# Kernel tuning notes

Measured on AMD Instinct MI355X. Metric: run time of the kernel, lower is better.

## Reference

```python
import jax, jax.numpy as jnp
from jax import lax
import numpy as np

B = 2048
N = 10  # wires on q_device0
C64 = jnp.complex64

# fixed gate matrices (qubit ordering matches wire-list order)
S_ = jnp.array([[1, 0], [0, 1j]], C64)
T_ = jnp.array([[1, 0], [0, np.exp(1j * np.pi / 4)]], C64)
SX_ = 0.5 * jnp.array([[1 + 1j, 1 - 1j], [1 - 1j, 1 + 1j]], C64)
Y_ = jnp.array([[0, -1j], [1j, 0]], C64)
CNOT_ = jnp.array([[1, 0, 0, 0], [0, 1, 0, 0], [0, 0, 0, 1], [0, 0, 1, 0]], C64)
CZ_ = jnp.diag(jnp.array([1, 1, 1, -1], C64))
CY_ = jnp.array([[1, 0, 0, 0], [0, 1, 0, 0], [0, 0, 0, -1j], [0, 0, 1j, 0]], C64)
SWAP_ = jnp.array([[1, 0, 0, 0], [0, 0, 1, 0], [0, 1, 0, 0], [0, 0, 0, 1]], C64)
_cs = np.eye(8); _cs[[5, 6]] = _cs[[6, 5]]  # CSWAP: |101> <-> |110>
CSWAP_ = jnp.array(_cs, C64)
_tf = np.eye(8); _tf[[6, 7]] = _tf[[7, 6]]  # Toffoli: |110> <-> |111>
TOFF_ = jnp.array(_tf, C64)

# parametrized single-qubit gate builders; t scalar -> [2,2], t [B] -> [B,2,2]
def _rx(t):
    c = jnp.cos(t / 2).astype(C64)
    s = -1j * jnp.sin(t / 2).astype(C64)
    return jnp.stack([jnp.stack([c, s], -1), jnp.stack([s, c], -1)], -2)

def _ry(t):
    c = jnp.cos(t / 2).astype(C64)
    s = jnp.sin(t / 2).astype(C64)
    return jnp.stack([jnp.stack([c, -s], -1), jnp.stack([s, c], -1)], -2)

def _rz(t):
    a = jnp.exp(-0.5j * t.astype(C64))
    b = jnp.exp(0.5j * t.astype(C64))
    z = jnp.zeros_like(a)
    return jnp.stack([jnp.stack([a, z], -1), jnp.stack([z, b], -1)], -2)

def _phase(t):
    e = jnp.exp(1j * t.astype(C64))
    o = jnp.ones_like(e)
    z = jnp.zeros_like(e)
    return jnp.stack([jnp.stack([o, z], -1), jnp.stack([z, e], -1)], -2)

def _rot(phi, th, om):  # RZ(om) RY(th) RZ(phi), pennylane/torchquantum convention
    c = jnp.cos(th / 2).astype(C64)
    s = jnp.sin(th / 2).astype(C64)
    p = phi.astype(C64); w = om.astype(C64)
    m00 = jnp.exp(-0.5j * (p + w)) * c
    m01 = -jnp.exp(0.5j * (p - w)) * s
    m10 = jnp.exp(-0.5j * (p - w)) * s
    m11 = jnp.exp(0.5j * (p + w)) * c
    return jnp.stack([jnp.stack([m00, m01], -1), jnp.stack([m10, m11], -1)], -2)

def _apply1(psi, U, w):  # psi: [B]+(2,)*N, U: [2,2] or [B,2,2]
    s = jnp.moveaxis(psi, w + 1, 1)
    if U.ndim == 2:
        s = jnp.einsum('ij,bj...->bi...', U, s)
    else:
        s = jnp.einsum('bij,bj...->bi...', U, s)
    return jnp.moveaxis(s, 1, w + 1)

def _applyk(psi, U, wires):  # fixed k-qubit gate, U: [2^k, 2^k]
    k = len(wires)
    axes = tuple(w + 1 for w in wires)
    s = jnp.moveaxis(psi, axes, tuple(range(1, k + 1)))
    sh = s.shape
    s = s.reshape((sh[0], 2 ** k) + sh[k + 1:])
    s = jnp.einsum('ij,bj...->bi...', U, s)
    return jnp.moveaxis(s.reshape(sh), tuple(range(1, k + 1)), axes)

def _forward(x, conv1_w, conv1_b, conv2_w, conv2_b, fc1_w, fc1_b, fc2_w, fc2_b,
             theta0, theta_rz, theta_ps, rot_p):
    dn = ('NCHW', 'OIHW', 'NCHW')
    h = lax.conv_general_dilated(x, conv1_w, (1, 1), 'VALID', dimension_numbers=dn)
    h = jax.nn.relu(h + conv1_b[None, :, None, None])
    h = lax.conv_general_dilated(h, conv2_w, (1, 1), 'VALID', dimension_numbers=dn)
    h = jax.nn.relu(h + conv2_b[None, :, None, None])
    h = lax.reduce_window(h, -jnp.inf, lax.max, (1, 1, 2, 2), (1, 1, 2, 2), 'VALID')
    h = h.reshape(h.shape[0], -1)  # [B, 9216], dropout = identity (eval)
    h = jax.nn.relu(h @ fc1_w.T + fc1_b)
    a = jax.nn.sigmoid(h @ fc2_w.T + fc2_b) * (2.0 * np.pi)  # angles [B, 10]
    bsz = a.shape[0]
    psi = jnp.zeros((bsz, 2 ** N), C64).at[:, 0].set(1.0).reshape((bsz,) + (2,) * N)
    trz = jnp.reshape(theta_rz, ())
    tps = jnp.reshape(theta_ps, ())
    for k in range(N):                      # TrainableRxAll
        psi = _apply1(psi, _rx(theta0[k]), k)
    for k in range(N):                      # RxAll with input angles
        psi = _apply1(psi, _rx(a[:, k]), k)
    psi = _apply1(psi, _rx(a[:, 1]), 1)
    psi = _apply1(psi, _rx(jnp.asarray(-np.pi / 4, jnp.float32)), 5)  # q_layer2 fixed
    psi = _apply1(psi, _ry(a[:, 2]), 2)
    psi = _apply1(psi, _rz(a[:, 3]), 3)
    psi = _apply1(psi, S_, 4)
    psi = _apply1(psi, T_, 5)
    psi = _apply1(psi, _rz(trz), 6)         # q_layer3
    psi = _apply1(psi, SX_, 7)
    # (q_device1 ops on a separate 3-wire device do not affect the output)
    psi = _applyk(psi, CZ_, (0, 5))
    psi = _applyk(psi, CNOT_, (0, 5))
    psi = _applyk(psi, CY_, (0, 5))
    psi = _applyk(psi, CY_, (3, 8))         # q_layer4
    psi = _applyk(psi, SWAP_, (2, 3))
    psi = _applyk(psi, CSWAP_, (4, 5, 6))
    psi = _applyk(psi, TOFF_, (8, 5, 0))    # q_layer5
    psi = _apply1(psi, _phase(tps), 8)      # q_layer6
    psi = _apply1(psi, _phase(a[:, 7]), 7)
    psi = _apply1(psi, _rot(rot_p[0], rot_p[1], rot_p[2]), 4)  # q_layer7
    psi = _apply1(psi, _rot(a[:, 6], a[:, 7], a[:, 8]), 5)
    axes = tuple(range(1, N + 1))
    evs = [jnp.real(jnp.sum(jnp.conj(psi) * _apply1(psi, Y_, k), axis=axes))
           for k in range(N)]
    ev = jnp.stack(evs, -1)                 # [B, 10] <Y_k>
    return jax.nn.log_softmax(ev, axis=1)


def setup_inputs() -> dict:
    key = jax.random.key(0)
    ks = jax.random.split(key, 13)
    return {
        'x': jax.random.normal(ks[0], (B, 1, 28, 28), jnp.float32),
        'conv1_w': jax.random.normal(ks[1], (32, 1, 3, 3), jnp.float32) * 0.2,
        'conv1_b': jnp.zeros((32,), jnp.float32),
        'conv2_w': jax.random.normal(ks[2], (64, 32, 3, 3), jnp.float32) * 0.05,
        'conv2_b': jnp.zeros((64,), jnp.float32),
        'fc1_w': jax.random.normal(ks[3], (128, 9216), jnp.float32) * 0.01,
        'fc1_b': jnp.zeros((128,), jnp.float32),
        'fc2_w': jax.random.normal(ks[4], (10, 128), jnp.float32) * 0.1,
        'fc2_b': jnp.zeros((10,), jnp.float32),
        'theta0': jax.random.normal(ks[5], (10,), jnp.float32),
        'theta_rz': jax.random.normal(ks[6], (1,), jnp.float32),
        'theta_ps': jax.random.normal(ks[7], (1,), jnp.float32),
        'rot_p': jax.random.normal(ks[8], (3,), jnp.float32),
    }


def reference(x, conv1_w, conv1_b, conv2_w, conv2_b, fc1_w, fc1_b, fc2_w, fc2_b,
              theta0, theta_rz, theta_ps, rot_p):
    return _forward(x, conv1_w, conv1_b, conv2_w, conv2_b, fc1_w, fc1_b, fc2_w, fc2_b,
                    theta0, theta_rz, theta_ps, rot_p)
```

## Files before the change

kernel.cpp:

```cpp
#include <hip/hip_runtime.h>
#include <math.h>

typedef short short8 __attribute__((ext_vector_type(8)));
typedef float f32x4 __attribute__((ext_vector_type(4)));
typedef float f32x16 __attribute__((ext_vector_type(16)));

#define GLB_CP(p) ((const __attribute__((address_space(1))) void*)(p))
#define LDS_CP(p) ((__attribute__((address_space(3))) void*)(p))

__device__ __forceinline__ float2 cmul(float2 a, float2 b) {
    return make_float2(a.x * b.x - a.y * b.y, a.x * b.y + a.y * b.x);
}

__device__ __forceinline__ ushort f2bf(float f) {
    uint u = __float_as_uint(f);
    uint r = (u + 0x7FFFu + ((u >> 16) & 1u)) >> 16;
    return (ushort)r;
}

__global__ __launch_bounds__(256) void prep_kernel(
    const float* __restrict__ c2w, const float* __restrict__ f1w,
    ushort* __restrict__ wt2, ushort* __restrict__ wf1)
{
    int i = blockIdx.x * 256 + threadIdx.x;
    if (i < 18432) {
        int icl = i & 7;
        int t = i >> 3;
        int oc = t & 63;
        int t2 = t >> 6;
        int icg = t2 & 3;
        int tap = t2 >> 2;
        int ic = icg * 8 + icl;
        wt2[i] = f2bf(c2w[(oc * 32 + ic) * 9 + tap]);
    } else if (i < 18432 + 1179648) {
        int j = i - 18432;
        wf1[j] = f2bf(f1w[j]);
    }
}

__global__ __launch_bounds__(256) void conv1_kernel(
    const float* __restrict__ x, const float* __restrict__ w1,
    const float* __restrict__ b1, ushort* __restrict__ h1b)
{
    __shared__ float wl[288];
    __shared__ float bl[32];
    int tid = threadIdx.x;
    for (int e = tid; e < 288; e += 256) wl[e] = w1[e];
    if (tid < 32) bl[tid] = b1[tid];
    __syncthreads();
    int e = blockIdx.x * 256 + tid;
    int icg = e & 3;
    int t = e >> 2;
    int pix = t % 676;
    int b = t / 676;
    int y = pix / 26, xc = pix % 26;
    const float* xp = x + b * 784 + y * 28 + xc;
    float in9[9];
#pragma unroll
    for (int ky = 0; ky < 3; ++ky)
#pragma unroll
        for (int kx = 0; kx < 3; ++kx) in9[ky * 3 + kx] = xp[ky * 28 + kx];
    short8 outv;
#pragma unroll
    for (int o = 0; o < 8; ++o) {
        int oc = icg * 8 + o;
        float acc = bl[oc];
#pragma unroll
        for (int k = 0; k < 9; ++k) acc = fmaf(in9[k], wl[oc * 9 + k], acc);
        outv[o] = (short)f2bf(fmaxf(acc, 0.f));
    }
    *(short8*)&h1b[((b * 4 + icg) * 676 + pix) * 8] = outv;
}

__global__ __launch_bounds__(384, 3) void conv2_img(
    const ushort* __restrict__ h1b, const ushort* __restrict__ wt2,
    const float* __restrict__ c2b, ushort* __restrict__ pooled)
{
    __shared__ __attribute__((aligned(16))) ushort wt_lds[18432];
    __shared__ __attribute__((aligned(16))) ushort in_lds[2][8704];
    int b = blockIdx.x;
    int tid = threadIdx.x;
    int wave = tid >> 6;
    int lane = tid & 63;
    int lo = lane & 31;
    int hi = lane >> 5;

    for (int c = wave; c < 36; c += 6) {
        const ushort* src = wt2 + (size_t)(c * 64 + lane) * 8;
        __builtin_amdgcn_global_load_lds(GLB_CP(src), LDS_CP(wt_lds + c * 512), 16, 0, 0);
    }
    {
        const ushort* base = h1b + (size_t)b * 21632;
        for (int c = wave; c < 17; c += 6) {
            int e = c * 64 + lane;
            if (e > 1039) e = 1039;
            int icg = e / 260;
            int rem = e - icg * 260;
            const ushort* src = base + ((size_t)icg * 676 + rem) * 8;
            __builtin_amdgcn_global_load_lds(GLB_CP(src), LDS_CP(in_lds[0] + c * 512), 16, 0, 0);
        }
    }
    float bias0 = c2b[lo];
    float bias1 = c2b[lo + 32];
    __syncthreads();

    int rx = wave % 3, ry = wave / 3;
    int xcoord = rx * 8 + (lo & 7);
    int ycoord = ry * 4 + (lo >> 3);
    int pbase = ycoord * 26 + xcoord;
    ushort* pout = pooled + (size_t)b * 9216;
    int pcolb = rx * 4 + 2 * hi;

#pragma unroll
    for (int band = 0; band < 3; ++band) {
        if (band < 2) {
            const ushort* base = h1b + (size_t)b * 21632 + (size_t)(band + 1) * 8 * 26 * 8;
            ushort* dst = in_lds[(band + 1) & 1];
            for (int c = wave; c < 17; c += 6) {
                int e = c * 64 + lane;
                if (e > 1039) e = 1039;
                int icg = e / 260;
                int rem = e - icg * 260;
                const ushort* src = base + ((size_t)icg * 676 + rem) * 8;
                __builtin_amdgcn_global_load_lds(GLB_CP(src), LDS_CP(dst + c * 512), 16, 0, 0);
            }
        }

        const ushort* ib = in_lds[band & 1];
        f32x16 acc0 = (f32x16)0.f, acc1 = (f32x16)0.f;
#pragma unroll
        for (int tap = 0; tap < 9; ++tap) {
            int off = (tap / 3) * 26 + (tap % 3);
#pragma unroll
            for (int ks = 0; ks < 2; ++ks) {
                short8 bf = *(const short8*)&ib[((ks * 2 + hi) * 260 + pbase + off) * 8];
                short8 a0 = *(const short8*)&wt_lds[((tap * 4 + ks * 2 + hi) * 64 + lo) * 8];
                short8 a1 = *(const short8*)&wt_lds[((tap * 4 + ks * 2 + hi) * 64 + 32 + lo) * 8];
                acc0 = __builtin_amdgcn_mfma_f32_32x32x16_bf16(bf, a0, acc0, 0, 0, 0);
                acc1 = __builtin_amdgcn_mfma_f32_32x32x16_bf16(bf, a1, acc1, 0, 0, 0);
            }
        }

#pragma unroll
        for (int q = 0; q < 2; ++q) {
            int prow = band * 4 + ry * 2 + q;
            int base = 8 * q;
            float m00 = fmaxf(fmaxf(acc0[base], acc0[base + 1]), fmaxf(acc0[base + 4], acc0[base + 5]));
            float m01 = fmaxf(fmaxf(acc0[base + 2], acc0[base + 3]), fmaxf(acc0[base + 6], acc0[base + 7]));
            uint pk0 = (uint)f2bf(fmaxf(m00 + bias0, 0.f)) | ((uint)f2bf(fmaxf(m01 + bias0, 0.f)) << 16);
            *(uint*)&pout[lo * 144 + prow * 12 + pcolb] = pk0;
            float m10 = fmaxf(fmaxf(acc1[base], acc1[base + 1]), fmaxf(acc1[base + 4], acc1[base + 5]));
            float m11 = fmaxf(fmaxf(acc1[base + 2], acc1[base + 3]), fmaxf(acc1[base + 6], acc1[base + 7]));
            uint pk1 = (uint)f2bf(fmaxf(m10 + bias1, 0.f)) | ((uint)f2bf(fmaxf(m11 + bias1, 0.f)) << 16);
            *(uint*)&pout[(lo + 32) * 144 + prow * 12 + pcolb] = pk1;
        }
        __syncthreads();
    }
}

__global__ __launch_bounds__(256) void fc1_mfma(
    const ushort* __restrict__ pooled, const ushort* __restrict__ wf1,
    float* __restrict__ part)
{
    int bx = blockIdx.x, by = blockIdx.y;
    int tid = threadIdx.x;
    int wid = tid >> 6, lane = tid & 63;
    int lo = lane & 15, hi = lane >> 4;
    int m0 = bx * 32;
    int kb = by * 2304;

    f32x4 acc[2][2];
#pragma unroll
    for (int mt = 0; mt < 2; ++mt)
#pragma unroll
        for (int j = 0; j < 2; ++j) acc[mt][j] = (f32x4)0.f;

    const ushort* arow0 = pooled + (size_t)(m0 + lo) * 9216 + kb + hi * 8;
    const ushort* arow1 = arow0 + 16 * 9216;
    const ushort* brow0 = wf1 + (size_t)(wid * 32 + lo) * 9216 + kb + hi * 8;
    const ushort* brow1 = brow0 + 16 * 9216;

    for (int kt = 0; kt < 72; ++kt) {
        short8 a0 = *(const short8*)(arow0 + kt * 32);
        short8 a1 = *(const short8*)(arow1 + kt * 32);
        short8 b0 = *(const short8*)(brow0 + kt * 32);
        short8 b1 = *(const short8*)(brow1 + kt * 32);
        acc[0][0] = __builtin_amdgcn_mfma_f32_16x16x32_bf16(a0, b0, acc[0][0], 0, 0, 0);
        acc[1][0] = __builtin_amdgcn_mfma_f32_16x16x32_bf16(a1, b0, acc[1][0], 0, 0, 0);
        acc[0][1] = __builtin_amdgcn_mfma_f32_16x16x32_bf16(a0, b1, acc[0][1], 0, 0, 0);
        acc[1][1] = __builtin_amdgcn_mfma_f32_16x16x32_bf16(a1, b1, acc[1][1], 0, 0, 0);
    }
    float* pp = part + (size_t)by * 262144;
#pragma unroll
    for (int mt = 0; mt < 2; ++mt)
#pragma unroll
        for (int j = 0; j < 2; ++j)
#pragma unroll
            for (int r = 0; r < 4; ++r)
                pp[(m0 + mt * 16 + hi * 4 + r) * 128 + wid * 32 + j * 16 + lo] = acc[mt][j][r];
}

__global__ __launch_bounds__(256) void fc1_reduce_kernel(
    const float* __restrict__ part, const float* __restrict__ bias,
    float* __restrict__ outp)
{
    int idx = blockIdx.x * 256 + threadIdx.x;
    float s = 0.f;
#pragma unroll
    for (int ks = 0; ks < 4; ++ks) s += part[ks * 262144 + idx];
    outp[idx] = fmaxf(s + bias[idx & 127], 0.f);
}

__global__ __launch_bounds__(256) void fc2_kernel(
    const float* __restrict__ h, const float* __restrict__ w,
    const float* __restrict__ bias, float* __restrict__ ang)
{
    int idx = blockIdx.x * 256 + threadIdx.x;
    if (idx >= 20480) return;
    int b = idx / 10, n = idx % 10;
    const float* hp = h + b * 128;
    const float* wp = w + n * 128;
    float s = bias[n];
    for (int k = 0; k < 128; ++k) s = fmaf(hp[k], wp[k], s);
    ang[idx] = 6.28318530718f / (1.f + expf(-s));
}

__device__ __forceinline__ void apply_rot(float2* s, int p, float phi, float th,
                                          float om, int tid)
{
    float c, sn; sincosf(0.5f * th, &sn, &c);
    float A = 0.5f * (phi + om), Bv = 0.5f * (phi - om);
    float cA, sA; sincosf(A, &sA, &cA);
    float cB, sB; sincosf(Bv, &sB, &cB);
    float2 m00 = make_float2(cA * c, -sA * c);
    float2 m01 = make_float2(-cB * sn, -sB * sn);
    float2 m10 = make_float2(cB * sn, -sB * sn);
    float2 m11 = make_float2(cA * c, sA * c);
    for (int q = tid; q < 512; q += 256) {
        int i0 = ((q >> p) << (p + 1)) | (q & ((1 << p) - 1));
        int i1 = i0 | (1 << p);
        float2 aa = s[i0], bb = s[i1];
        s[i0] = make_float2(m00.x * aa.x - m00.y * aa.y + m01.x * bb.x - m01.y * bb.y,
                            m00.x * aa.y + m00.y * aa.x + m01.x * bb.y + m01.y * bb.x);
        s[i1] = make_float2(m10.x * aa.x - m10.y * aa.y + m11.x * bb.x - m11.y * bb.y,
                            m10.x * aa.y + m10.y * aa.x + m11.x * bb.y + m11.y * bb.x);
    }
}

__global__ __launch_bounds__(256) void quantum_kernel(
    const float* __restrict__ ang, const float* __restrict__ theta0,
    const float* __restrict__ theta_rz, const float* __restrict__ theta_ps,
    const float* __restrict__ rot_p, float* __restrict__ out)
{
    __shared__ float2 s[1024];
    __shared__ float red[40];
    int b = blockIdx.x;
    int tid = threadIdx.x;

    float a[10];
#pragma unroll
    for (int k = 0; k < 10; ++k) a[k] = ang[b * 10 + k];
    float th[10];
#pragma unroll
    for (int k = 0; k < 10; ++k) th[k] = theta0[k] + a[k];
    th[1] += a[1];
    th[5] -= 0.78539816339745f;

    float2 v[10][2];
#pragma unroll
    for (int k = 0; k < 10; ++k) {
        float c, sn; sincosf(0.5f * th[k], &sn, &c);
        v[k][0] = make_float2(c, 0.f);
        v[k][1] = make_float2(0.f, -sn);
    }
    { float c, sn; sincosf(0.5f * a[2], &sn, &c);
      float2 v0 = v[2][0], v1 = v[2][1];
      v[2][0] = make_float2(c * v0.x - sn * v1.x, c * v0.y - sn * v1.y);
      v[2][1] = make_float2(sn * v0.x + c * v1.x, sn * v0.y + c * v1.y); }
    { float c, sn; sincosf(0.5f * a[3], &sn, &c);
      v[3][0] = cmul(v[3][0], make_float2(c, -sn));
      v[3][1] = cmul(v[3][1], make_float2(c, sn)); }
    { float2 t = v[4][1]; v[4][1] = make_float2(-t.y, t.x); }
    { const float r = 0.70710678118655f;
      float2 t = v[5][1]; v[5][1] = make_float2(r * (t.x - t.y), r * (t.x + t.y)); }
    { float c, sn; sincosf(0.5f * theta_rz[0], &sn, &c);
      v[6][0] = cmul(v[6][0], make_float2(c, -sn));
      v[6][1] = cmul(v[6][1], make_float2(c, sn)); }
    { float2 p = v[7][0], q = v[7][1];
      v[7][0] = make_float2(0.5f * ((p.x - p.y) + (q.x + q.y)),
                            0.5f * ((p.x + p.y) + (q.y - q.x)));
      v[7][1] = make_float2(0.5f * ((p.x + p.y) + (q.x - q.y)),
                            0.5f * ((p.y - p.x) + (q.x + q.y))); }

    for (int i = tid; i < 1024; i += 256) {
        float2 c = ((i >> 9) & 1) ? v[0][1] : v[0][0];
#pragma unroll
        for (int k = 1; k < 10; ++k) {
            float2 vk = ((i >> (9 - k)) & 1) ? v[k][1] : v[k][0];
            c = cmul(c, vk);
        }
        s[i] = c;
    }
    __syncthreads();

    for (int i = tid; i < 1024; i += 256)
        if (((i >> 9) & 1) && ((i >> 4) & 1)) { s[i].x = -s[i].x; s[i].y = -s[i].y; }
    __syncthreads();
    { int j = tid;
      int i0 = 512 | ((j >> 4) << 5) | (j & 15);
      int i1 = i0 | 16;
      float2 t0 = s[i0], t1 = s[i1];
      s[i0] = t1; s[i1] = t0; }
    __syncthreads();
    { int j = tid;
      int i0 = 512 | ((j >> 4) << 5) | (j & 15);
      int i1 = i0 | 16;
      float2 t0 = s[i0], t1 = s[i1];
      s[i0] = make_float2(t1.y, -t1.x);
      s[i1] = make_float2(-t0.y, t0.x); }
    __syncthreads();
    { int j = tid;
      int i0 = (j & 1) | (((j >> 1) & 15) << 2) | (((j >> 5) & 7) << 7) | 64;
      int i1 = i0 | 2;
      float2 t0 = s[i0], t1 = s[i1];
      s[i0] = make_float2(t1.y, -t1.x);
      s[i1] = make_float2(-t0.y, t0.x); }
    __syncthreads();
    { int j = tid;
      int i0 = (j & 63) | 128 | (((j >> 6) & 3) << 8);
      int i1 = i0 ^ 0xC0;
      float2 t0 = s[i0], t1 = s[i1];
      s[i0] = t1; s[i1] = t0; }
    __syncthreads();
    if (tid < 128) {
      int j = tid;
      int i0 = (j & 7) | 16 | 32 | (((j >> 3) & 15) << 6);
      int i1 = i0 ^ 0x18;
      float2 t0 = s[i0], t1 = s[i1];
      s[i0] = t1; s[i1] = t0; }
    __syncthreads();
    if (tid < 128) {
      int j = tid;
      int i0 = (j & 1) | 2 | (((j >> 1) & 3) << 2) | 16 | (((j >> 3) & 15) << 5);
      int i1 = i0 | 512;
      float2 t0 = s[i0], t1 = s[i1];
      s[i0] = t1; s[i1] = t0; }
    __syncthreads();
    { float c1, s1; sincosf(theta_ps[0], &s1, &c1);
      float c2, s2; sincosf(a[7], &s2, &c2);
      float2 p1 = make_float2(c1, s1), p2 = make_float2(c2, s2);
      for (int i = tid; i < 1024; i += 256) {
          float2 t = s[i];
          if ((i >> 1) & 1) t = cmul(t, p1);
          if ((i >> 2) & 1) t = cmul(t, p2);
          s[i] = t;
      } }
    __syncthreads();
    apply_rot(s, 5, rot_p[0], rot_p[1], rot_p[2], tid);
    __syncthreads();
    apply_rot(s, 4, a[6], a[7], a[8], tid);
    __syncthreads();

    int wave = tid >> 6;
    for (int k = 0; k < 10; ++k) {
        int p = 9 - k;
        float part = 0.f;
        for (int q = tid; q < 512; q += 256) {
            int i0 = ((q >> p) << (p + 1)) | (q & ((1 << p) - 1));
            int i1 = i0 | (1 << p);
            float2 aa = s[i0], bb = s[i1];
            part += aa.x * bb.y - aa.y * bb.x;
        }
        part *= 2.f;
#pragma unroll
        for (int off = 32; off > 0; off >>= 1)
            part += __shfl_down(part, off, 64);
        if ((tid & 63) == 0) red[k * 4 + wave] = part;
    }
    __syncthreads();
    if (tid == 0) {
        float ev[10];
        float mx = -1e30f;
#pragma unroll
        for (int k = 0; k < 10; ++k) {
            ev[k] = red[k * 4] + red[k * 4 + 1] + red[k * 4 + 2] + red[k * 4 + 3];
            mx = fmaxf(mx, ev[k]);
        }
        float sum = 0.f;
#pragma unroll
        for (int k = 0; k < 10; ++k) sum += expf(ev[k] - mx);
        float lse = mx + logf(sum);
#pragma unroll
        for (int k = 0; k < 10; ++k) out[b * 10 + k] = ev[k] - lse;
    }
}

extern "C" void kernel_launch(void* const* d_in, const int* in_sizes, int n_in,
                              void* d_out, int out_size, void* d_ws, size_t ws_size,
                              hipStream_t stream)
{
    (void)in_sizes; (void)n_in; (void)out_size; (void)ws_size;
    const float* x    = (const float*)d_in[0];
    const float* c1w  = (const float*)d_in[1];
    const float* c1b  = (const float*)d_in[2];
    const float* c2w  = (const float*)d_in[3];
    const float* c2b  = (const float*)d_in[4];
    const float* f1w  = (const float*)d_in[5];
    const float* f1b  = (const float*)d_in[6];
    const float* f2w  = (const float*)d_in[7];
    const float* f2b  = (const float*)d_in[8];
    const float* th0  = (const float*)d_in[9];
    const float* trz  = (const float*)d_in[10];
    const float* tps  = (const float*)d_in[11];
    const float* rotp = (const float*)d_in[12];
    float* out = (float*)d_out;

    char* ws = (char*)d_ws;
    ushort* h1b    = (ushort*)(ws);
    ushort* pooled = (ushort*)(ws + 88604672);
    ushort* wt2    = (ushort*)(ws + 126353408);
    ushort* wf1    = (ushort*)(ws + 126390272);
    float*  part   = (float*)(ws + 128749568);
    float*  fc1o   = (float*)(ws + 132943872);
    float*  ang    = (float*)(ws + 133992448);

    prep_kernel<<<4680, 256, 0, stream>>>(c2w, f1w, wt2, wf1);
    conv1_kernel<<<21632, 256, 0, stream>>>(x, c1w, c1b, h1b);
    conv2_img<<<2048, 384, 0, stream>>>(h1b, wt2, c2b, pooled);
    fc1_mfma<<<dim3(64, 4), 256, 0, stream>>>(pooled, wf1, part);
    fc1_reduce_kernel<<<1024, 256, 0, stream>>>(part, f1b, fc1o);
    fc2_kernel<<<80, 256, 0, stream>>>(fc1o, f2w, f2b, ang);
    quantum_kernel<<<2048, 256, 0, stream>>>(ang, th0, trz, tps, rotp, out);
}
```

Before: 161.0 us.

## Make conv2 persistent over 8 images per block with whole-image LDS tiles

The conv2 kernel now launches 256 blocks that each loop over 8 images, loading the weights into LDS once per block instead of once per image. Each iteration double-buffers a full 26x26x32 input image, in place of three row bands, and each wave computes three 32-pixel tiles so the weight fragments it reads are reused across six MFMAs. This cuts repeated weight loads and per-band synchronisation, but uses more LDS and more accumulator registers (occupancy hint drops to 2). It also leaves 256 blocks to cover the whole GPU, which may underfill the CUs.

```diff
diff --git a/kernel.cpp b/kernel.cpp
--- a/kernel.cpp
+++ b/kernel.cpp
@@ -72,13 +72,31 @@
     *(short8*)&h1b[((b * 4 + icg) * 676 + pix) * 8] = outv;
 }
 
-__global__ __launch_bounds__(384, 3) void conv2_img(
+#define EPILOG(ACC0, ACC1, RX, RY)                                                         \
+    {                                                                                      \
+        int pcolb = (RX) * 4 + 2 * hi;                                                     \
+        _Pragma("unroll")                                                                  \
+        for (int q = 0; q < 2; ++q) {                                                      \
+            int prow = (RY) * 2 + q;                                                       \
+            int bs = 8 * q;                                                                \
+            float m00 = fmaxf(fmaxf(ACC0[bs], ACC0[bs + 1]), fmaxf(ACC0[bs + 4], ACC0[bs + 5])); \
+            float m01 = fmaxf(fmaxf(ACC0[bs + 2], ACC0[bs + 3]), fmaxf(ACC0[bs + 6], ACC0[bs + 7])); \
+            uint pk0 = (uint)f2bf(fmaxf(m00 + bias0, 0.f)) | ((uint)f2bf(fmaxf(m01 + bias0, 0.f)) << 16); \
+            *(uint*)&pout[lo * 144 + prow * 12 + pcolb] = pk0;                             \
+            float m10 = fmaxf(fmaxf(ACC1[bs], ACC1[bs + 1]), fmaxf(ACC1[bs + 4], ACC1[bs + 5])); \
+            float m11 = fmaxf(fmaxf(ACC1[bs + 2], ACC1[bs + 3]), fmaxf(ACC1[bs + 6], ACC1[bs + 7])); \
+            uint pk1 = (uint)f2bf(fmaxf(m10 + bias1, 0.f)) | ((uint)f2bf(fmaxf(m11 + bias1, 0.f)) << 16); \
+            *(uint*)&pout[(lo + 32) * 144 + prow * 12 + pcolb] = pk1;                      \
+        }                                                                                  \
+    }
+
+__global__ __launch_bounds__(384, 2) void conv2_persist(
     const ushort* __restrict__ h1b, const ushort* __restrict__ wt2,
     const float* __restrict__ c2b, ushort* __restrict__ pooled)
 {
     __shared__ __attribute__((aligned(16))) ushort wt_lds[18432];
-    __shared__ __attribute__((aligned(16))) ushort in_lds[2][8704];
-    int b = blockIdx.x;
+    __shared__ __attribute__((aligned(16))) ushort in_lds[2][22016];
+    int cu = blockIdx.x;
     int tid = threadIdx.x;
     int wave = tid >> 6;
     int lane = tid & 63;
@@ -90,70 +108,73 @@
         __builtin_amdgcn_global_load_lds(GLB_CP(src), LDS_CP(wt_lds + c * 512), 16, 0, 0);
     }
     {
-        const ushort* base = h1b + (size_t)b * 21632;
-        for (int c = wave; c < 17; c += 6) {
+        const ushort* base = h1b + (size_t)(cu * 8) * 21632;
+        for (int c = wave; c < 43; c += 6) {
             int e = c * 64 + lane;
-            if (e > 1039) e = 1039;
-            int icg = e / 260;
-            int rem = e - icg * 260;
-            const ushort* src = base + ((size_t)icg * 676 + rem) * 8;
-            __builtin_amdgcn_global_load_lds(GLB_CP(src), LDS_CP(in_lds[0] + c * 512), 16, 0, 0);
+            if (e > 2703) e = 2703;
+            __builtin_amdgcn_global_load_lds(GLB_CP(base + (size_t)e * 8),
+                                             LDS_CP(in_lds[0] + c * 512), 16, 0, 0);
         }
     }
     float bias0 = c2b[lo];
     float bias1 = c2b[lo + 32];
     __syncthreads();
 
-    int rx = wave % 3, ry = wave / 3;
-    int xcoord = rx * 8 + (lo & 7);
-    int ycoord = ry * 4 + (lo >> 3);
-    int pbase = ycoord * 26 + xcoord;
-    ushort* pout = pooled + (size_t)b * 9216;
-    int pcolb = rx * 4 + 2 * hi;
-
-#pragma unroll
-    for (int band = 0; band < 3; ++band) {
-        if (band < 2) {
-            const ushort* base = h1b + (size_t)b * 21632 + (size_t)(band + 1) * 8 * 26 * 8;
-            ushort* dst = in_lds[(band + 1) & 1];
-            for (int c = wave; c < 17; c += 6) {
+    int pb[3];
+#pragma unroll
+    for (int i = 0; i < 3; ++i) {
+        int r = wave + 6 * i;
+        int rx = r % 3, ry = r / 3;
+        int xcoord = rx * 8 + (lo & 7);
+        int ycoord = ry * 4 + (lo >> 3);
+        pb[i] = ycoord * 26 + xcoord;
+    }
+    int rx0 = wave % 3, ry0 = wave / 3;
+    int rx1 = (wave + 6) % 3, ry1 = (wave + 6) / 3;
+    int rx2 = (wave + 12) % 3, ry2 = (wave + 12) / 3;
+
+    for (int j = 0; j < 8; ++j) {
+        if (j < 7) {
+            const ushort* base = h1b + (size_t)(cu * 8 + j + 1) * 21632;
+            ushort* dst = in_lds[(j + 1) & 1];
+            for (int c = wave; c < 43; c += 6) {
                 int e = c * 64 + lane;
-                if (e > 1039) e = 1039;
-                int icg = e / 260;
-                int rem = e - icg * 260;
-                const ushort* src = base + ((size_t)icg * 676 + rem) * 8;
-                __builtin_amdgcn_global_load_lds(GLB_CP(src), LDS_CP(dst + c * 512), 16, 0, 0);
+                if (e > 2703) e = 2703;
+                __builtin_amdgcn_global_load_lds(GLB_CP(base + (size_t)e * 8),
+                                                 LDS_CP(dst + c * 512), 16, 0, 0);
             }
         }
 
-        const ushort* ib = in_lds[band & 1];
-        f32x16 acc0 = (f32x16)0.f, acc1 = (f32x16)0.f;
+        const ushort* ib = in_lds[j & 1];
+        f32x16 aA0 = (f32x16)0.f, aA1 = (f32x16)0.f;
+        f32x16 aB0 = (f32x16)0.f, aB1 = (f32x16)0.f;
+        f32x16 aC0 = (f32x16)0.f, aC1 = (f32x16)0.f;
+
 #pragma unroll
         for (int tap = 0; tap < 9; ++tap) {
             int off = (tap / 3) * 26 + (tap % 3);
 #pragma unroll
             for (int ks = 0; ks < 2; ++ks) {
-                short8 bf = *(const short8*)&ib[((ks * 2 + hi) * 260 + pbase + off) * 8];
-                short8 a0 = *(const short8*)&wt_lds[((tap * 4 + ks * 2 + hi) * 64 + lo) * 8];
-                short8 a1 = *(const short8*)&wt_lds[((tap * 4 + ks * 2 + hi) * 64 + 32 + lo) * 8];
-                acc0 = __builtin_amdgcn_mfma_f32_32x32x16_bf16(bf, a0, acc0, 0, 0, 0);
-                acc1 = __builtin_amdgcn_mfma_f32_32x32x16_bf16(bf, a1, acc1, 0, 0, 0);
+                const ushort* wp = &wt_lds[((tap * 4 + ks * 2 + hi) * 64) * 8];
+                short8 a0 = *(const short8*)(wp + lo * 8);
+                short8 a1 = *(const short8*)(wp + (32 + lo) * 8);
+                const ushort* ip = &ib[((ks * 2 + hi) * 676 + off) * 8];
+                short8 b0 = *(const short8*)(ip + pb[0] * 8);
+                short8 b1 = *(const short8*)(ip + pb[1] * 8);
+                short8 b2 = *(const short8*)(ip + pb[2] * 8);
+                aA0 = __builtin_amdgcn_mfma_f32_32x32x16_bf16(b0, a0, aA0, 0, 0, 0);
+                aA1 = __builtin_amdgcn_mfma_f32_32x32x16_bf16(b0, a1, aA1, 0, 0, 0);
+                aB0 = __builtin_amdgcn_mfma_f32_32x32x16_bf16(b1, a0, aB0, 0, 0, 0);
+                aB1 = __builtin_amdgcn_mfma_f32_32x32x16_bf16(b1, a1, aB1, 0, 0, 0);
+                aC0 = __builtin_amdgcn_mfma_f32_32x32x16_bf16(b2, a0, aC0, 0, 0, 0);
+                aC1 = __builtin_amdgcn_mfma_f32_32x32x16_bf16(b2, a1, aC1, 0, 0, 0);
             }
         }
 
-#pragma unroll
-        for (int q = 0; q < 2; ++q) {
-            int prow = band * 4 + ry * 2 + q;
-            int base = 8 * q;
-            float m00 = fmaxf(fmaxf(acc0[base], acc0[base + 1]), fmaxf(acc0[base + 4], acc0[base + 5]));
-            float m01 = fmaxf(fmaxf(acc0[base + 2], acc0[base + 3]), fmaxf(acc0[base + 6], acc0[base + 7]));
-            uint pk0 = (uint)f2bf(fmaxf(m00 + bias0, 0.f)) | ((uint)f2bf(fmaxf(m01 + bias0, 0.f)) << 16);
-            *(uint*)&pout[lo * 144 + prow * 12 + pcolb] = pk0;
-            float m10 = fmaxf(fmaxf(acc1[base], acc1[base + 1]), fmaxf(acc1[base + 4], acc1[base + 5]));
-            float m11 = fmaxf(fmaxf(acc1[base + 2], acc1[base + 3]), fmaxf(acc1[base + 6], acc1[base + 7]));
-            uint pk1 = (uint)f2bf(fmaxf(m10 + bias1, 0.f)) | ((uint)f2bf(fmaxf(m11 + bias1, 0.f)) << 16);
-            *(uint*)&pout[(lo + 32) * 144 + prow * 12 + pcolb] = pk1;
-        }
+        ushort* pout = pooled + (size_t)(cu * 8 + j) * 9216;
+        EPILOG(aA0, aA1, rx0, ry0)
+        EPILOG(aB0, aB1, rx1, ry1)
+        EPILOG(aC0, aC1, rx2, ry2)
         __syncthreads();
     }
 }
@@ -426,7 +447,7 @@
 
     prep_kernel<<<4680, 256, 0, stream>>>(c2w, f1w, wt2, wf1);
     conv1_kernel<<<21632, 256, 0, stream>>>(x, c1w, c1b, h1b);
-    conv2_img<<<2048, 384, 0, stream>>>(h1b, wt2, c2b, pooled);
+    conv2_persist<<<256, 384, 0, stream>>>(h1b, wt2, c2b, pooled);
     fc1_mfma<<<dim3(64, 4), 256, 0, stream>>>(pooled, wf1, part);
     fc1_reduce_kernel<<<1024, 256, 0, stream>>>(part, f1b, fc1o);
     fc2_kernel<<<80, 256, 0, stream>>>(fc1o, f2w, f2b, ang);
```

Result: faster. 155.0 us (-3.7%).
